# Kernel tuning notes

Hardware: AMD Instinct MI355X
Metric: run time of the kernel (lower is better)

The kernel has to match this reference:

```python
import jax, jax.numpy as jnp
import numpy as np

N, D, H, E, K = 16384, 1024, 4096, 8, 2
EPS = 1e-5


def setup_inputs() -> dict:
    key = jax.random.key(0)
    ks = jax.random.split(key, 12)
    s = 0.02
    return {
        "x": jax.random.normal(ks[0], (N, D), dtype=jnp.float32),
        "ln_g": jnp.ones((D,), jnp.float32),
        "ln_b": jnp.zeros((D,), jnp.float32),
        "r_w1": jax.random.normal(ks[1], (D, H // 2), jnp.float32) * s,
        "r_b1": jnp.zeros((H // 2,), jnp.float32),
        "r_w2": jax.random.normal(ks[2], (H // 2, E), jnp.float32) * s,
        "r_b2": jnp.zeros((E,), jnp.float32),
        "e_w1": jax.random.normal(ks[3], (E, D, H), jnp.float32) * s,
        "e_b1": jnp.zeros((E, H), jnp.float32),
        "e_w2": jax.random.normal(ks[4], (E, H, D), jnp.float32) * s,
        "e_b2": jnp.zeros((E, D), jnp.float32),
    }


def reference(x, ln_g, ln_b, r_w1, r_b1, r_w2, r_b2, e_w1, e_b1, e_w2, e_b2):
    # LayerNorm
    mu = jnp.mean(x, axis=-1, keepdims=True)
    var = jnp.mean(jnp.square(x - mu), axis=-1, keepdims=True)
    xn = (x - mu) * jax.lax.rsqrt(var + EPS) * ln_g + ln_b  # [N, D]

    # Router: Linear -> ReLU -> Linear -> softmax -> top-k, renormalize
    logits = jax.nn.relu(xn @ r_w1 + r_b1) @ r_w2 + r_b2  # [N, E]
    probs = jax.nn.softmax(logits, axis=-1)
    vals, idx = jax.lax.top_k(probs, K)  # [N, K]
    vals = vals / jnp.sum(vals, axis=-1, keepdims=True)

    # Dense expert dispatch: loop over fixed small E, weight by combine gate
    out = jnp.zeros_like(x)
    for e in range(E):
        gate = jnp.sum(vals * (idx == e).astype(vals.dtype), axis=-1)  # [N]
        h = jax.nn.relu(xn @ e_w1[e] + e_b1[e])  # dropout in eval mode -> identity
        y = h @ e_w2[e] + e_b2[e]  # [N, D]
        out = out + gate[:, None] * y
    return x + out
```

## Files before the change

kernel.cpp:

```cpp
#include <hip/hip_runtime.h>
#include <cstdint>
#include <cstddef>

typedef unsigned short u16;
typedef __attribute__((ext_vector_type(8))) short bf16x8;
typedef __attribute__((ext_vector_type(4))) float f32x4;

#define N_TOK 16384
#define DIM   1024
#define HID   4096
#define NEXP  8
#define HR    2048
#define TAU   0.02f
#define MAXMT 264

__device__ __forceinline__ u16 f2bf(float f) {
  union { float f; uint32_t u; } x; x.f = f;
  uint32_t r = x.u + 0x7FFFu + ((x.u >> 16) & 1u);
  return (u16)(r >> 16);
}
__device__ __forceinline__ float bf2f(u16 u) {
  union { uint32_t u; float f; } x; x.u = ((uint32_t)u) << 16; return x.f;
}

__device__ __forceinline__ void async16(const void* g, const void* l) {
  auto gp = reinterpret_cast<const __attribute__((address_space(1))) uint32_t*>(
      reinterpret_cast<uintptr_t>(g));
  auto lp = reinterpret_cast<__attribute__((address_space(3))) uint32_t*>(
      reinterpret_cast<uintptr_t>(l));
  __builtin_amdgcn_global_load_lds(gp, lp, 16, 0, 0);
}

__device__ __forceinline__ unsigned xcd_swz(unsigned flat, unsigned nwg) {
  const unsigned xcd = flat & 7u, lid = flat >> 3;
  const unsigned q = nwg >> 3, r = nwg & 7u;
  return (xcd < r ? xcd * (q + 1u) : r * (q + 1u) + (xcd - r) * q) + lid;
}

template<bool SPLIT>
__global__ __launch_bounds__(256)
void transpose_cvt(const float* __restrict__ src, u16* __restrict__ hi,
                   u16* __restrict__ lo, int R, int C)
{
  __shared__ float tile[32][33];
  const size_t bofs = (size_t)blockIdx.z * R * C;
  src += bofs; hi += bofs; if (SPLIT) lo += bofs;
  const int tx = threadIdx.x, ty = threadIdx.y;
  const int c0 = blockIdx.x * 32, r0 = blockIdx.y * 32;
#pragma unroll
  for (int i = 0; i < 4; ++i)
    tile[ty + i * 8][tx] = src[(size_t)(r0 + ty + i * 8) * C + c0 + tx];
  __syncthreads();
#pragma unroll
  for (int i = 0; i < 4; ++i) {
    float v = tile[tx][ty + i * 8];
    size_t o = (size_t)(c0 + ty + i * 8) * R + r0 + tx;
    u16 h = f2bf(v);
    hi[o] = h;
    if (SPLIT) lo[o] = f2bf(v - bf2f(h));
  }
}

__global__ __launch_bounds__(256)
void ln_kernel(const float* __restrict__ x, const float* __restrict__ g,
               const float* __restrict__ b, u16* __restrict__ xh,
               u16* __restrict__ xl, float* __restrict__ out)
{
  const int row = blockIdx.x;
  const int t = threadIdx.x;
  const float4 xv = ((const float4*)(x + (size_t)row * DIM))[t];
  float s = xv.x + xv.y + xv.z + xv.w;
  float q = xv.x * xv.x + xv.y * xv.y + xv.z * xv.z + xv.w * xv.w;
#pragma unroll
  for (int off = 32; off; off >>= 1) {
    s += __shfl_down(s, off, 64);
    q += __shfl_down(q, off, 64);
  }
  __shared__ float sm[8];
  __shared__ float mu_s, rs_s;
  const int lane = t & 63, wv = t >> 6;
  if (lane == 0) { sm[wv] = s; sm[wv + 4] = q; }
  __syncthreads();
  if (t == 0) {
    float S = sm[0] + sm[1] + sm[2] + sm[3];
    float Q = sm[4] + sm[5] + sm[6] + sm[7];
    float mu = S * (1.f / DIM);
    float var = Q * (1.f / DIM) - mu * mu;
    mu_s = mu; rs_s = rsqrtf(var + 1e-5f);
  }
  __syncthreads();
  const float mu = mu_s, rs = rs_s;
  const float4 gv = ((const float4*)g)[t];
  const float4 bv = ((const float4*)b)[t];
  float n0 = (xv.x - mu) * rs * gv.x + bv.x;
  float n1 = (xv.y - mu) * rs * gv.y + bv.y;
  float n2 = (xv.z - mu) * rs * gv.z + bv.z;
  float n3 = (xv.w - mu) * rs * gv.w + bv.w;
  ushort4 h, l;
  h.x = f2bf(n0); l.x = f2bf(n0 - bf2f(h.x));
  h.y = f2bf(n1); l.y = f2bf(n1 - bf2f(h.y));
  h.z = f2bf(n2); l.z = f2bf(n2 - bf2f(h.z));
  h.w = f2bf(n3); l.w = f2bf(n3 - bf2f(h.w));
  ((ushort4*)(xh + (size_t)row * DIM))[t] = h;
  ((ushort4*)(xl + (size_t)row * DIM))[t] = l;
  ((float4*)(out + (size_t)row * DIM))[t] = xv;
}

__global__ __launch_bounds__(256)
void logits_kernel(const u16* __restrict__ HrB, const float* __restrict__ w2,
                   float* __restrict__ logits)
{
  const int row = blockIdx.x, t = threadIdx.x;
  const u16* h = HrB + (size_t)row * HR;
  const ushort4* hv = (const ushort4*)(h + t * 8);
  ushort4 h0 = hv[0], h1 = hv[1];
  u16 hh[8] = {h0.x, h0.y, h0.z, h0.w, h1.x, h1.y, h1.z, h1.w};
  float p[8] = {0, 0, 0, 0, 0, 0, 0, 0};
#pragma unroll
  for (int j = 0; j < 8; ++j) {
    const int col = t * 8 + j;
    const float v = bf2f(hh[j]);
    const float4* wp = (const float4*)(w2 + (size_t)col * 8);
    float4 a = wp[0], b = wp[1];
    p[0] += v * a.x; p[1] += v * a.y; p[2] += v * a.z; p[3] += v * a.w;
    p[4] += v * b.x; p[5] += v * b.y; p[6] += v * b.z; p[7] += v * b.w;
  }
#pragma unroll
  for (int off = 32; off; off >>= 1)
#pragma unroll
    for (int e = 0; e < 8; ++e) p[e] += __shfl_down(p[e], off, 64);
  __shared__ float sm[4][8];
  const int lane = t & 63, wv = t >> 6;
  if (lane == 0) {
#pragma unroll
    for (int e = 0; e < 8; ++e) sm[wv][e] = p[e];
  }
  __syncthreads();
  if (t < 8)
    logits[(size_t)row * 8 + t] = sm[0][t] + sm[1][t] + sm[2][t] + sm[3][t];
}

__device__ __forceinline__ void load_logits(const float* logits, const float* b2,
                                            int row, float l[8]) {
  const float4* lp = (const float4*)(logits + (size_t)row * 8);
  float4 a = lp[0], b = lp[1];
  l[0] = a.x + b2[0]; l[1] = a.y + b2[1]; l[2] = a.z + b2[2]; l[3] = a.w + b2[3];
  l[4] = b.x + b2[4]; l[5] = b.y + b2[5]; l[6] = b.z + b2[6]; l[7] = b.w + b2[7];
}
__device__ __forceinline__ void top2(const float l[8], int& i0, float& l0,
                                     int& i1, float& l1) {
  i0 = 0; l0 = l[0];
#pragma unroll
  for (int e = 1; e < 8; ++e) if (l[e] > l0) { l0 = l[e]; i0 = e; }
  i1 = -1; l1 = -1e30f;
#pragma unroll
  for (int e = 0; e < 8; ++e) if (e != i0 && l[e] > l1) { l1 = l[e]; i1 = e; }
}

__global__ __launch_bounds__(256)
void pass_flag(float* __restrict__ logits, const float* __restrict__ b2,
               int* __restrict__ fixL, int* __restrict__ cntFix)
{
  __shared__ int lcnt;
  __shared__ int base;
  const int t = threadIdx.x;
  const int row = blockIdx.x * 256 + t;
  if (t == 0) lcnt = 0;
  float l[8]; load_logits(logits, b2, row, l);
  int i0, i1; float l0, l1;
  top2(l, i0, l0, i1, l1);
  float l2 = -1e30f;
#pragma unroll
  for (int e = 0; e < 8; ++e)
    if (e != i0 && e != i1 && l[e] > l2) l2 = l[e];
  const bool flag = (l1 - l2) < TAU;
  __syncthreads();
  int r = 0;
  if (flag) r = atomicAdd(&lcnt, 1);
  __syncthreads();
  if (t == 0) base = atomicAdd(cntFix, lcnt);
  __syncthreads();
  if (flag) {
    fixL[base + r] = row;
    float4 z = {0.f, 0.f, 0.f, 0.f};
    ((float4*)(logits + (size_t)row * 8))[0] = z;
    ((float4*)(logits + (size_t)row * 8))[1] = z;
  }
}

__global__ __launch_bounds__(256)
void pass_count(const float* __restrict__ logits, const float* __restrict__ b2,
                int* __restrict__ cnts)
{
  __shared__ int lcnt[NEXP];
  const int t = threadIdx.x;
  const int row = blockIdx.x * 256 + t;
  if (t < NEXP) lcnt[t] = 0;
  float l[8]; load_logits(logits, b2, row, l);
  int i0, i1; float l0, l1;
  top2(l, i0, l0, i1, l1);
  __syncthreads();
  atomicAdd(&lcnt[i0], 1);
  atomicAdd(&lcnt[i1], 1);
  __syncthreads();
  if (t < NEXP) atomicAdd(&cnts[t], lcnt[t]);
}

__global__ void scan_kernel(const int* __restrict__ cnts, int* __restrict__ offs,
                            int* __restrict__ tileOffs)
{
  if (threadIdx.x == 0) {
    int s = 0, ts = 0;
#pragma unroll
    for (int e = 0; e < NEXP; ++e) {
      offs[e] = s; s += cnts[e];
      tileOffs[e] = ts; ts += (cnts[e] + 127) >> 7;
    }
    offs[NEXP] = s;
    tileOffs[NEXP] = ts;
  }
}

__global__ __launch_bounds__(256)
void pass_scatter(const float* __restrict__ logits, const float* __restrict__ b2,
                  const int* __restrict__ offs, int* __restrict__ cnts2,
                  int* __restrict__ rowsC, float* __restrict__ gateC)
{
  __shared__ int lcnt[NEXP];
  __shared__ int sbase[NEXP];
  const int t = threadIdx.x;
  const int row = blockIdx.x * 256 + t;
  if (t < NEXP) lcnt[t] = 0;
  float l[8]; load_logits(logits, b2, row, l);
  int i0, i1; float l0, l1;
  top2(l, i0, l0, i1, l1);
  float tt = expf(l1 - l0);
  float g0 = 1.f / (1.f + tt);
  float g1 = tt / (1.f + tt);
  __syncthreads();
  int r0 = atomicAdd(&lcnt[i0], 1);
  int r1 = atomicAdd(&lcnt[i1], 1);
  __syncthreads();
  if (t < NEXP) sbase[t] = atomicAdd(&cnts2[t], lcnt[t]);
  __syncthreads();
  int p0 = offs[i0] + sbase[i0] + r0;
  int p1 = offs[i1] + sbase[i1] + r1;
  rowsC[p0] = row; gateC[p0] = g0;
  rowsC[p1] = row; gateC[p1] = g1;
}

template<int EPI, bool GATHER, bool DENSE>
__global__ __launch_bounds__(256, 3)
void gemm_moe(const u16* __restrict__ A0, const u16* __restrict__ B0,
              int lda, int ldb, int K, int NT, int Mdense,
              size_t bStrideE, int biasStrideE,
              const int* __restrict__ counts,
              const int* __restrict__ offs, const int* __restrict__ tileOffs,
              const int* __restrict__ rowsC, const float* __restrict__ gatesC,
              const float* __restrict__ bias,
              u16* __restrict__ Cbf, float* __restrict__ Cf32, int ldc)
{
  const unsigned swz = xcd_swz(blockIdx.x, gridDim.x);
  const int mt = (int)(swz / (unsigned)NT);
  int e, m0, Mq, off;
  if constexpr (DENSE) {
    if (mt >= Mdense / 128) return;
    e = 0; m0 = mt * 128; Mq = Mdense; off = 0;
  } else {
    if (mt >= tileOffs[NEXP]) return;
    e = 0;
#pragma unroll
    for (int i = 1; i < NEXP; ++i) if (tileOffs[i] <= mt) e = i;
    m0 = (mt - tileOffs[e]) * 128;
    Mq = counts[e];
    if (m0 >= Mq) return;
    off = offs[e];
  }
  const int n0 = (int)(swz % (unsigned)NT) * 128;
  const int* rows = DENSE ? nullptr : (rowsC + off);
  const u16* B = B0 + (size_t)e * bStrideE;
  const float* bi = bias + (size_t)e * biasStrideE;

  __shared__ alignas(16) u16 As[3][128 * 32];
  __shared__ alignas(16) u16 Bs[3][128 * 32];

  const int t = threadIdx.x;
  const int numK = K >> 5;

  const u16* aptr[2]; const u16* bptr[2]; int sdst[2];
#pragma unroll
  for (int i = 0; i < 2; ++i) {
    const int gdx = i * 256 + t;
    const int r = gdx >> 2;
    const int cb = ((gdx & 3) << 4) ^ (((gdx >> 5) & 1) << 5);
    const int cs = cb >> 1;
    int amc = (m0 + r) < Mq ? (m0 + r) : (Mq - 1);
    const size_t agr = DENSE ? (size_t)(m0 + r)
                             : (GATHER ? (size_t)rows[amc] : (size_t)(off + amc));
    aptr[i] = A0 + agr * lda + cs;
    bptr[i] = B + (size_t)(n0 + r) * ldb + cs;
    sdst[i] = gdx * 8;
  }

  const int lane = t & 63, wv = t >> 6;
  const int wm = wv >> 1;
  const int wn = wv & 1;
  const int fr = lane & 15, fq = lane >> 4;

  int aIdx[4], bIdx[4];
#pragma unroll
  for (int mf = 0; mf < 4; ++mf) {
    const int r = wm * 64 + mf * 16 + fr;
    aIdx[mf] = r * 32 + ((fq * 8) ^ (((r >> 3) & 1) << 4));
  }
#pragma unroll
  for (int nf = 0; nf < 4; ++nf) {
    const int rb = wn * 64 + nf * 16 + fr;
    bIdx[nf] = rb * 32 + ((fq * 8) ^ (((rb >> 3) & 1) << 4));
  }

  f32x4 acc[4][4];
#pragma unroll
  for (int i = 0; i < 4; ++i)
#pragma unroll
    for (int j = 0; j < 4; ++j) acc[i][j] = (f32x4){0.f, 0.f, 0.f, 0.f};

#pragma unroll
  for (int h = 0; h < 2; ++h) {
    async16(bptr[0] + h * 32, &Bs[h][sdst[0]]);
    async16(bptr[1] + h * 32, &Bs[h][sdst[1]]);
    async16(aptr[0] + h * 32, &As[h][sdst[0]]);
    async16(aptr[1] + h * 32, &As[h][sdst[1]]);
  }
  asm volatile("s_waitcnt vmcnt(4)" ::: "memory");
  __builtin_amdgcn_s_barrier();
  __builtin_amdgcn_sched_barrier(0);

  int sR = 0;
  int sW = 2;
  for (int T = 0; T < numK; ++T) {
    if (T + 2 < numK) {
      async16(bptr[0] + (size_t)(T + 2) * 32, &Bs[sW][sdst[0]]);
      async16(bptr[1] + (size_t)(T + 2) * 32, &Bs[sW][sdst[1]]);
      async16(aptr[0] + (size_t)(T + 2) * 32, &As[sW][sdst[0]]);
      async16(aptr[1] + (size_t)(T + 2) * 32, &As[sW][sdst[1]]);
    }

    const u16* aL = As[sR];
    const u16* bL = Bs[sR];
    bf16x8 aF[4], bF[4];
#pragma unroll
    for (int i = 0; i < 4; ++i) {
      aF[i] = *(const bf16x8*)&aL[aIdx[i]];
      bF[i] = *(const bf16x8*)&bL[bIdx[i]];
    }
    __builtin_amdgcn_s_setprio(1);
#pragma unroll
    for (int mf = 0; mf < 4; ++mf)
#pragma unroll
      for (int nf = 0; nf < 4; ++nf)
        acc[mf][nf] = __builtin_amdgcn_mfma_f32_16x16x32_bf16(
            aF[mf], bF[nf], acc[mf][nf], 0, 0, 0);
    __builtin_amdgcn_s_setprio(0);
    __builtin_amdgcn_sched_barrier(0);

    const int rem = numK - T;
    if (rem >= 3) {
      asm volatile("s_waitcnt vmcnt(4)" ::: "memory");
      __builtin_amdgcn_s_barrier();
      __builtin_amdgcn_sched_barrier(0);
    } else if (rem == 2) {
      asm volatile("s_waitcnt vmcnt(0)" ::: "memory");
      __builtin_amdgcn_s_barrier();
      __builtin_amdgcn_sched_barrier(0);
    }

    sR = (sR == 2) ? 0 : sR + 1;
    sW = (sW == 2) ? 0 : sW + 1;
  }

  float bv[4];
#pragma unroll
  for (int nf = 0; nf < 4; ++nf) bv[nf] = bi[n0 + wn * 64 + nf * 16 + fr];

#pragma unroll
  for (int mf = 0; mf < 4; ++mf)
#pragma unroll
    for (int r = 0; r < 4; ++r) {
      const int m = m0 + wm * 64 + mf * 16 + fq * 4 + r;
      if (m < Mq) {
        if constexpr (EPI == 2) {
          const size_t orow = (size_t)rows[m];
          const float g = gatesC[off + m];
#pragma unroll
          for (int nf = 0; nf < 4; ++nf) {
            const int n = n0 + wn * 64 + nf * 16 + fr;
            atomicAdd(&Cf32[orow * ldc + n], g * (acc[mf][nf][r] + bv[nf]));
          }
        } else {
#pragma unroll
          for (int nf = 0; nf < 4; ++nf) {
            const int n = n0 + wn * 64 + nf * 16 + fr;
            Cbf[(size_t)(off + m) * ldc + n] =
                f2bf(fmaxf(acc[mf][nf][r] + bv[nf], 0.f));
          }
        }
      }
    }
}

template<bool SPLIT, int EPI, bool GATHER>
__global__ __launch_bounds__(256, 2)
void gemm_bt(const u16* __restrict__ A0, const u16* __restrict__ A1,
             const u16* __restrict__ B0, const u16* __restrict__ B1,
             int lda, int ldb, int K, int M,
             const int* __restrict__ counts, int expertArg,
             const int* __restrict__ offs,
             const int* __restrict__ rowsC, const float* __restrict__ gatesC,
             const float* __restrict__ bias,
             const float* __restrict__ w2, float* __restrict__ logits,
             u16* __restrict__ Cbf, float* __restrict__ Cf32, int ldc)
{
  int expert, m0, n0;
  if (counts == nullptr) {
    const unsigned nwg = gridDim.x * gridDim.y;
    const unsigned flat = blockIdx.y * gridDim.x + blockIdx.x;
    const unsigned swz = xcd_swz(flat, nwg);
    expert = expertArg;
    m0 = (int)(swz / gridDim.x) * 128;
    n0 = (int)(swz % gridDim.x) * 128;
  } else {
    expert = expertArg;
    m0 = blockIdx.y * 128;
    n0 = blockIdx.x * 128;
  }

  const int Mq = counts ? counts[expert] : M;
  if (m0 >= Mq) return;
  const int off = offs ? offs[expert] : 0;
  const int* rows = rowsC ? rowsC + off : nullptr;
  const float* gates = gatesC ? gatesC + off : nullptr;
  const u16* B = B0;
  const u16* Bl = SPLIT ? B1 : nullptr;
  const float* bi = bias;
  const int z = (int)blockIdx.z;
  const int zOff = z * K;

  __shared__ u16 As0[128 * 32], Bs0[128 * 32];
  __shared__ u16 As1[SPLIT ? 128 * 32 : 8], Bs1[SPLIT ? 128 * 32 : 8];

  const int t = threadIdx.x;
  size_t aoff[2]; int acodd[2]; size_t boff[2];
#pragma unroll
  for (int i = 0; i < 2; ++i) {
    int gdx = i * 256 + t;
    int ar = gdx >> 2, ac = (gdx & 3) * 8;
    int am = m0 + ar;
    int amc = am < Mq ? am : (Mq - 1);
    int agr = GATHER ? rows[amc] : amc;
    aoff[i] = (size_t)agr * lda + ac + zOff;
    boff[i] = (size_t)(n0 + ar) * ldb + ac + zOff;
    acodd[i] = gdx * 8;
  }

  f32x4 acc[4][4];
#pragma unroll
  for (int i = 0; i < 4; ++i)
#pragma unroll
    for (int j = 0; j < 4; ++j) acc[i][j] = (f32x4){0.f, 0.f, 0.f, 0.f};

  const int lane = t & 63, wv = t >> 6;
  const int wm = (wv >> 1) * 64, wn = (wv & 1) * 64;
  const int fr = lane & 15, fq = lane >> 4;

  for (int k0 = 0; k0 < K; k0 += 32) {
    __syncthreads();
#pragma unroll
    for (int i = 0; i < 2; ++i) {
      async16(A0 + aoff[i] + k0, &As0[acodd[i]]);
      async16(B + boff[i] + k0, &Bs0[acodd[i]]);
      if (SPLIT) {
        async16(A1 + aoff[i] + k0, &As1[acodd[i]]);
        async16(Bl + boff[i] + k0, &Bs1[acodd[i]]);
      }
    }
    __syncthreads();
    bf16x8 af[4], bfr[4], af1[4], bf1[4];
#pragma unroll
    for (int xi = 0; xi < 4; ++xi) {
      af[xi]  = *(const bf16x8*)&As0[(wm + xi * 16 + fr) * 32 + fq * 8];
      bfr[xi] = *(const bf16x8*)&Bs0[(wn + xi * 16 + fr) * 32 + fq * 8];
      if (SPLIT) {
        af1[xi] = *(const bf16x8*)&As1[(wm + xi * 16 + fr) * 32 + fq * 8];
        bf1[xi] = *(const bf16x8*)&Bs1[(wn + xi * 16 + fr) * 32 + fq * 8];
      }
    }
#pragma unroll
    for (int mt = 0; mt < 4; ++mt)
#pragma unroll
      for (int nt = 0; nt < 4; ++nt) {
        acc[mt][nt] = __builtin_amdgcn_mfma_f32_16x16x32_bf16(af[mt], bfr[nt], acc[mt][nt], 0, 0, 0);
        if (SPLIT) {
          acc[mt][nt] = __builtin_amdgcn_mfma_f32_16x16x32_bf16(af[mt], bf1[nt], acc[mt][nt], 0, 0, 0);
          acc[mt][nt] = __builtin_amdgcn_mfma_f32_16x16x32_bf16(af1[mt], bfr[nt], acc[mt][nt], 0, 0, 0);
        }
      }
  }

  if constexpr (EPI == 3) {
    float w2v[4][8]; float b1v[4];
#pragma unroll
    for (int nt = 0; nt < 4; ++nt) {
      const int n = n0 + wn + nt * 16 + fr;
      b1v[nt] = bi[n];
      const float4* wp = (const float4*)(w2 + (size_t)n * 8);
      float4 wa = wp[0], wb = wp[1];
      w2v[nt][0] = wa.x; w2v[nt][1] = wa.y; w2v[nt][2] = wa.z; w2v[nt][3] = wa.w;
      w2v[nt][4] = wb.x; w2v[nt][5] = wb.y; w2v[nt][6] = wb.z; w2v[nt][7] = wb.w;
    }
#pragma unroll
    for (int mt = 0; mt < 4; ++mt) {
      float pe[4][8];
#pragma unroll
      for (int r = 0; r < 4; ++r)
#pragma unroll
        for (int ee = 0; ee < 8; ++ee) pe[r][ee] = 0.f;
#pragma unroll
      for (int nt = 0; nt < 4; ++nt)
#pragma unroll
        for (int r = 0; r < 4; ++r) {
          float v = fmaxf(acc[mt][nt][r] + b1v[nt], 0.f);
#pragma unroll
          for (int ee = 0; ee < 8; ++ee) pe[r][ee] += v * w2v[nt][ee];
        }
#pragma unroll
      for (int offx = 1; offx < 16; offx <<= 1)
#pragma unroll
        for (int r = 0; r < 4; ++r)
#pragma unroll
          for (int ee = 0; ee < 8; ++ee)
            pe[r][ee] += __shfl_xor(pe[r][ee], offx, 64);
      if (fr == 0) {
#pragma unroll
        for (int r = 0; r < 4; ++r) {
          const int m = m0 + wm + mt * 16 + fq * 4 + r;
          if (m < Mq) {
            const int lrow = GATHER ? rows[m] : m;
#pragma unroll
            for (int ee = 0; ee < 8; ++ee)
              atomicAdd(&logits[(size_t)lrow * 8 + ee], pe[r][ee]);
          }
        }
      }
    }
    return;
  }

#pragma unroll
  for (int mt = 0; mt < 4; ++mt) {
#pragma unroll
    for (int nt = 0; nt < 4; ++nt) {
      const int n = n0 + wn + nt * 16 + fr;
      const float bvv = (z == 0) ? bi[n] : 0.f;
#pragma unroll
      for (int r = 0; r < 4; ++r) {
        const int m = m0 + wm + mt * 16 + fq * 4 + r;
        if (m < Mq) {
          float v = acc[mt][nt][r] + bvv;
          if constexpr (EPI == 1) {
            Cbf[(size_t)m * ldc + n] = f2bf(fmaxf(v, 0.f));
          } else {
            atomicAdd(&Cf32[(size_t)rows[m] * ldc + n], gates[m] * v);
          }
        }
      }
    }
  }
}

extern "C" void kernel_launch(void* const* d_in, const int* in_sizes, int n_in,
                              void* d_out, int out_size, void* d_ws, size_t ws_size,
                              hipStream_t stream)
{
  const float* x    = (const float*)d_in[0];
  const float* ln_g = (const float*)d_in[1];
  const float* ln_b = (const float*)d_in[2];
  const float* r_w1 = (const float*)d_in[3];
  const float* r_b1 = (const float*)d_in[4];
  const float* r_w2 = (const float*)d_in[5];
  const float* r_b2 = (const float*)d_in[6];
  const float* e_w1 = (const float*)d_in[7];
  const float* e_b1 = (const float*)d_in[8];
  const float* e_w2 = (const float*)d_in[9];
  const float* e_b2 = (const float*)d_in[10];
  float* out = (float*)d_out;

  char* ws = (char*)d_ws;
  const size_t MB = 1024ull * 1024ull;
  u16*   xnhi = (u16*)(ws);
  u16*   xnlo = (u16*)(ws + 32 * MB);
  u16*   rw1h = (u16*)(ws + 64 * MB);
  u16*   rw1l = (u16*)(ws + 68 * MB);
  u16*   ew1t = (u16*)(ws + 72 * MB);
  u16*   ew2t = (u16*)(ws + 136 * MB);
  float* logits = (float*)(ws + 200 * MB);
  int*   rowsC  = (int*)(ws + 200 * MB + 512 * 1024);
  float* gateC  = (float*)(ws + 200 * MB + 640 * 1024);
  int*   fixL   = (int*)(ws + 200 * MB + 768 * 1024);
  int*   cntb   = (int*)(ws + 200 * MB + 832 * 1024);
  int*   cnts   = cntb;
  int*   cnts2  = cntb + 8;
  int*   offs   = cntb + 16;
  int*   cntFix = cntb + 25;
  int*   tileOffs = cntb + 32;
  u16*   Hbuf = (u16*)(ws + 201 * MB);
  u16*   HrB  = Hbuf;
  (void)in_sizes; (void)n_in; (void)out_size;

  const bool fused = ws_size >= 458ull * MB;

  hipMemsetAsync(cntb, 0, 256, stream);

  dim3 tb(32, 8);
  transpose_cvt<true ><<<dim3(HR / 32, DIM / 32, 1), tb, 0, stream>>>(r_w1, rw1h, rw1l, DIM, HR);
  transpose_cvt<false><<<dim3(HID / 32, DIM / 32, NEXP), tb, 0, stream>>>(e_w1, ew1t, nullptr, DIM, HID);
  transpose_cvt<false><<<dim3(DIM / 32, HID / 32, NEXP), tb, 0, stream>>>(e_w2, ew2t, nullptr, HID, DIM);

  ln_kernel<<<N_TOK, 256, 0, stream>>>(x, ln_g, ln_b, xnhi, xnlo, out);

  gemm_moe<1, false, true><<<dim3((HR / 128) * (N_TOK / 128)), 256, 0, stream>>>(
      xnhi, rw1h, DIM, DIM, DIM, HR / 128, N_TOK, 0, 0,
      nullptr, nullptr, nullptr, nullptr, nullptr, r_b1,
      HrB, nullptr, HR);

  logits_kernel<<<N_TOK, 256, 0, stream>>>(HrB, r_w2, logits);

  pass_flag<<<N_TOK / 256, 256, 0, stream>>>(logits, r_b2, fixL, cntFix);

  gemm_bt<true, 3, true><<<dim3(HR / 128, N_TOK / 128), 256, 0, stream>>>(
      xnhi, xnlo, rw1h, rw1l, DIM, DIM, DIM, N_TOK,
      cntFix, 0, nullptr, fixL, nullptr, r_b1, r_w2, logits,
      nullptr, nullptr, 0);

  pass_count<<<N_TOK / 256, 256, 0, stream>>>(logits, r_b2, cnts);
  scan_kernel<<<1, 64, 0, stream>>>(cnts, offs, tileOffs);
  pass_scatter<<<N_TOK / 256, 256, 0, stream>>>(logits, r_b2, offs, cnts2, rowsC, gateC);

  if (fused) {
    gemm_moe<1, true, false><<<dim3((HID / 128) * MAXMT), 256, 0, stream>>>(
        xnhi, ew1t, DIM, DIM, DIM, HID / 128, 0,
        (size_t)HID * DIM, HID,
        cnts, offs, tileOffs, rowsC, nullptr, e_b1,
        Hbuf, nullptr, HID);
    gemm_moe<2, false, false><<<dim3((DIM / 128) * MAXMT), 256, 0, stream>>>(
        Hbuf, ew2t, HID, HID, HID, DIM / 128, 0,
        (size_t)DIM * HID, DIM,
        cnts, offs, tileOffs, rowsC, gateC, e_b2,
        nullptr, out, DIM);
  } else {
    for (int e = 0; e < NEXP; ++e) {
      gemm_bt<false, 1, true><<<dim3(HID / 128, N_TOK / 128), 256, 0, stream>>>(
          xnhi, nullptr, ew1t + (size_t)e * HID * DIM, nullptr,
          DIM, DIM, DIM, N_TOK,
          cnts, e, offs, rowsC, nullptr, e_b1 + (size_t)e * HID, nullptr, nullptr,
          Hbuf, nullptr, HID);
      gemm_bt<false, 2, false><<<dim3(DIM / 128, N_TOK / 128, 2), 256, 0, stream>>>(
          Hbuf, nullptr, ew2t + (size_t)e * DIM * HID, nullptr,
          HID, HID, HID / 2, N_TOK,
          cnts, e, offs, rowsC, gateC, e_b2 + (size_t)e * DIM, nullptr, nullptr,
          nullptr, out, DIM);
    }
  }
}
```

Before: 1.445 ms.

## Replace 128x128 MoE GEMM with 256x256 8-wave ping-pong pipelined kernel

Swaps the 128x128-tile, 4-wave GEMM used for the router first layer and both expert GEMMs for a 256x256-tile, 512-thread kernel with K-step 64 and double-buffered LDS split into halves. The loop interleaves quarter-tile MFMA groups with async loads of the next tiles, separated by barriers, and a second tile-offset table is added for 256-row expert tiles. The aim is more data reuse per byte loaded and better overlap of loads with MFMA. The cost is more padding waste on partial expert tiles, fewer blocks in the grid, and higher register and LDS pressure.

```diff
diff --git a/kernel.cpp b/kernel.cpp
--- a/kernel.cpp
+++ b/kernel.cpp
@@ -13,6 +13,7 @@
 #define HR    2048
 #define TAU   0.02f
 #define MAXMT 264
+#define MAXMT2 136
 
 __device__ __forceinline__ u16 f2bf(float f) {
   union { float f; uint32_t u; } x; x.f = f;
@@ -207,17 +208,19 @@
 }
 
 __global__ void scan_kernel(const int* __restrict__ cnts, int* __restrict__ offs,
-                            int* __restrict__ tileOffs)
+                            int* __restrict__ tileOffs, int* __restrict__ tileOffs2)
 {
   if (threadIdx.x == 0) {
-    int s = 0, ts = 0;
+    int s = 0, ts = 0, ts2 = 0;
 #pragma unroll
     for (int e = 0; e < NEXP; ++e) {
       offs[e] = s; s += cnts[e];
       tileOffs[e] = ts; ts += (cnts[e] + 127) >> 7;
+      tileOffs2[e] = ts2; ts2 += (cnts[e] + 255) >> 8;
     }
     offs[NEXP] = s;
     tileOffs[NEXP] = ts;
+    tileOffs2[NEXP] = ts2;
   }
 }
 
@@ -249,159 +252,202 @@
   rowsC[p1] = row; gateC[p1] = g1;
 }
 
+#define G8_BAR() do { __builtin_amdgcn_s_barrier(); \
+                      __builtin_amdgcn_sched_barrier(0); } while (0)
+#define G8_VM4() asm volatile("s_waitcnt vmcnt(4)" ::: "memory")
+#define G8_VM0() asm volatile("s_waitcnt vmcnt(0)" ::: "memory")
+
+#define READ_A(aL, mfh, Af) do { \
+  _Pragma("unroll") for (int mf = 0; mf < 4; ++mf) { \
+    Af[mf][0] = *(const bf16x8*)&(aL)[((mfh)*4+mf)*1024 + aBase + swzC[0]]; \
+    Af[mf][1] = *(const bf16x8*)&(aL)[((mfh)*4+mf)*1024 + aBase + swzC[1]]; \
+  } } while (0)
+
+#define READ_B(bL, nfh, Bf) do { \
+  _Pragma("unroll") for (int nf = 0; nf < 2; ++nf) { \
+    Bf[nf][0] = *(const bf16x8*)&(bL)[((nfh)*2+nf)*1024 + bBase + swzC[0]]; \
+    Bf[nf][1] = *(const bf16x8*)&(bL)[((nfh)*2+nf)*1024 + bBase + swzC[1]]; \
+  } } while (0)
+
+#define MFMA_Q(mfh, nfh, Af, Bf) do { \
+  __builtin_amdgcn_s_setprio(1); \
+  _Pragma("unroll") for (int mf = 0; mf < 4; ++mf) \
+  _Pragma("unroll") for (int nf = 0; nf < 2; ++nf) { \
+    acc[(mfh)*4+mf][(nfh)*2+nf] = __builtin_amdgcn_mfma_f32_16x16x32_bf16( \
+        Af[mf][0], Bf[nf][0], acc[(mfh)*4+mf][(nfh)*2+nf], 0, 0, 0); \
+    acc[(mfh)*4+mf][(nfh)*2+nf] = __builtin_amdgcn_mfma_f32_16x16x32_bf16( \
+        Af[mf][1], Bf[nf][1], acc[(mfh)*4+mf][(nfh)*2+nf], 0, 0, 0); \
+  } \
+  __builtin_amdgcn_s_setprio(0); } while (0)
+
 template<int EPI, bool GATHER, bool DENSE>
-__global__ __launch_bounds__(256, 3)
-void gemm_moe(const u16* __restrict__ A0, const u16* __restrict__ B0,
-              int lda, int ldb, int K, int NT, int Mdense,
-              size_t bStrideE, int biasStrideE,
-              const int* __restrict__ counts,
-              const int* __restrict__ offs, const int* __restrict__ tileOffs,
-              const int* __restrict__ rowsC, const float* __restrict__ gatesC,
-              const float* __restrict__ bias,
-              u16* __restrict__ Cbf, float* __restrict__ Cf32, int ldc)
+__global__ __launch_bounds__(512, 2)
+void gemm8p(const u16* __restrict__ A0, const u16* __restrict__ B0,
+            int lda, int ldb, int K, int NT, int Mdense,
+            size_t bStrideE, int biasStrideE,
+            const int* __restrict__ counts, const int* __restrict__ offs,
+            const int* __restrict__ tileOffs,
+            const int* __restrict__ rowsC, const float* __restrict__ gatesC,
+            const float* __restrict__ bias,
+            u16* __restrict__ Cbf, float* __restrict__ Cf32, int ldc)
 {
   const unsigned swz = xcd_swz(blockIdx.x, gridDim.x);
   const int mt = (int)(swz / (unsigned)NT);
   int e, m0, Mq, off;
   if constexpr (DENSE) {
-    if (mt >= Mdense / 128) return;
-    e = 0; m0 = mt * 128; Mq = Mdense; off = 0;
+    if (mt >= Mdense / 256) return;
+    e = 0; m0 = mt * 256; Mq = Mdense; off = 0;
   } else {
     if (mt >= tileOffs[NEXP]) return;
     e = 0;
 #pragma unroll
     for (int i = 1; i < NEXP; ++i) if (tileOffs[i] <= mt) e = i;
-    m0 = (mt - tileOffs[e]) * 128;
+    m0 = (mt - tileOffs[e]) * 256;
     Mq = counts[e];
     if (m0 >= Mq) return;
     off = offs[e];
   }
-  const int n0 = (int)(swz % (unsigned)NT) * 128;
+  const int n0 = (int)(swz % (unsigned)NT) * 256;
   const int* rows = DENSE ? nullptr : (rowsC + off);
   const u16* B = B0 + (size_t)e * bStrideE;
   const float* bi = bias + (size_t)e * biasStrideE;
 
-  __shared__ alignas(16) u16 As[3][128 * 32];
-  __shared__ alignas(16) u16 Bs[3][128 * 32];
+  __shared__ alignas(16) u16 As[2][2][128 * 64];
+  __shared__ alignas(16) u16 Bs[2][2][128 * 64];
 
   const int t = threadIdx.x;
-  const int numK = K >> 5;
-
-  const u16* aptr[2]; const u16* bptr[2]; int sdst[2];
-#pragma unroll
-  for (int i = 0; i < 2; ++i) {
-    const int gdx = i * 256 + t;
-    const int r = gdx >> 2;
-    const int cb = ((gdx & 3) << 4) ^ (((gdx >> 5) & 1) << 5);
-    const int cs = cb >> 1;
-    int amc = (m0 + r) < Mq ? (m0 + r) : (Mq - 1);
-    const size_t agr = DENSE ? (size_t)(m0 + r)
-                             : (GATHER ? (size_t)rows[amc] : (size_t)(off + amc));
-    aptr[i] = A0 + agr * lda + cs;
-    bptr[i] = B + (size_t)(n0 + r) * ldb + cs;
-    sdst[i] = gdx * 8;
-  }
+  const int numK = K >> 6;
+
+  const u16* aP[2][2]; const u16* bP[2][2]; int dst[2];
+#pragma unroll
+  for (int j = 0; j < 2; ++j) {
+    const int gdx = j * 512 + t;
+    const int rw = gdx >> 3;
+    const int cs = ((gdx & 7) ^ (rw & 7)) << 3;
+    dst[j] = gdx * 8;
+#pragma unroll
+    for (int h = 0; h < 2; ++h) {
+      const int grow = m0 + h * 128 + rw;
+      if constexpr (DENSE) {
+        aP[h][j] = A0 + (size_t)grow * lda + cs;
+      } else {
+        const int amc = grow < Mq ? grow : (Mq - 1);
+        const size_t agr = GATHER ? (size_t)rows[amc] : (size_t)(off + amc);
+        aP[h][j] = A0 + agr * lda + cs;
+      }
+      bP[h][j] = B + (size_t)(n0 + h * 128 + rw) * ldb + cs;
+    }
+  }
+
+  auto stA = [&](int tile, int h) {
+    async16(aP[h][0] + (size_t)tile * 64, &As[tile & 1][h][dst[0]]);
+    async16(aP[h][1] + (size_t)tile * 64, &As[tile & 1][h][dst[1]]);
+  };
+  auto stB = [&](int tile, int h) {
+    async16(bP[h][0] + (size_t)tile * 64, &Bs[tile & 1][h][dst[0]]);
+    async16(bP[h][1] + (size_t)tile * 64, &Bs[tile & 1][h][dst[1]]);
+  };
 
   const int lane = t & 63, wv = t >> 6;
-  const int wm = wv >> 1;
-  const int wn = wv & 1;
+  const int wr = wv >> 2;
+  const int wc = wv & 3;
   const int fr = lane & 15, fq = lane >> 4;
 
-  int aIdx[4], bIdx[4];
-#pragma unroll
-  for (int mf = 0; mf < 4; ++mf) {
-    const int r = wm * 64 + mf * 16 + fr;
-    aIdx[mf] = r * 32 + ((fq * 8) ^ (((r >> 3) & 1) << 4));
-  }
-#pragma unroll
-  for (int nf = 0; nf < 4; ++nf) {
-    const int rb = wn * 64 + nf * 16 + fr;
-    bIdx[nf] = rb * 32 + ((fq * 8) ^ (((rb >> 3) & 1) << 4));
-  }
-
-  f32x4 acc[4][4];
-#pragma unroll
-  for (int i = 0; i < 4; ++i)
+  int swzC[2];
+#pragma unroll
+  for (int ks = 0; ks < 2; ++ks)
+    swzC[ks] = ((ks * 4 + fq) ^ (fr & 7)) << 3;
+  const int aBase = fr * 64;
+  const int bBase = (wc & 1) * 4096 + fr * 64;
+
+  const u16* aH[2] = { &As[0][wr][0], &As[1][wr][0] };
+  const u16* bH[2] = { &Bs[0][wc >> 1][0], &Bs[1][wc >> 1][0] };
+
+  f32x4 acc[8][4];
+#pragma unroll
+  for (int i = 0; i < 8; ++i)
 #pragma unroll
     for (int j = 0; j < 4; ++j) acc[i][j] = (f32x4){0.f, 0.f, 0.f, 0.f};
 
-#pragma unroll
-  for (int h = 0; h < 2; ++h) {
-    async16(bptr[0] + h * 32, &Bs[h][sdst[0]]);
-    async16(bptr[1] + h * 32, &Bs[h][sdst[1]]);
-    async16(aptr[0] + h * 32, &As[h][sdst[0]]);
-    async16(aptr[1] + h * 32, &As[h][sdst[1]]);
-  }
-  asm volatile("s_waitcnt vmcnt(4)" ::: "memory");
-  __builtin_amdgcn_s_barrier();
-  __builtin_amdgcn_sched_barrier(0);
-
-  int sR = 0;
-  int sW = 2;
-  for (int T = 0; T < numK; ++T) {
-    if (T + 2 < numK) {
-      async16(bptr[0] + (size_t)(T + 2) * 32, &Bs[sW][sdst[0]]);
-      async16(bptr[1] + (size_t)(T + 2) * 32, &Bs[sW][sdst[1]]);
-      async16(aptr[0] + (size_t)(T + 2) * 32, &As[sW][sdst[0]]);
-      async16(aptr[1] + (size_t)(T + 2) * 32, &As[sW][sdst[1]]);
-    }
-
-    const u16* aL = As[sR];
-    const u16* bL = Bs[sR];
-    bf16x8 aF[4], bF[4];
-#pragma unroll
-    for (int i = 0; i < 4; ++i) {
-      aF[i] = *(const bf16x8*)&aL[aIdx[i]];
-      bF[i] = *(const bf16x8*)&bL[bIdx[i]];
-    }
-    __builtin_amdgcn_s_setprio(1);
-#pragma unroll
-    for (int mf = 0; mf < 4; ++mf)
-#pragma unroll
-      for (int nf = 0; nf < 4; ++nf)
-        acc[mf][nf] = __builtin_amdgcn_mfma_f32_16x16x32_bf16(
-            aF[mf], bF[nf], acc[mf][nf], 0, 0, 0);
-    __builtin_amdgcn_s_setprio(0);
-    __builtin_amdgcn_sched_barrier(0);
-
-    const int rem = numK - T;
-    if (rem >= 3) {
-      asm volatile("s_waitcnt vmcnt(4)" ::: "memory");
-      __builtin_amdgcn_s_barrier();
-      __builtin_amdgcn_sched_barrier(0);
-    } else if (rem == 2) {
-      asm volatile("s_waitcnt vmcnt(0)" ::: "memory");
-      __builtin_amdgcn_s_barrier();
-      __builtin_amdgcn_sched_barrier(0);
-    }
-
-    sR = (sR == 2) ? 0 : sR + 1;
-    sW = (sW == 2) ? 0 : sW + 1;
+  stB(0, 0); stB(0, 1); stA(0, 0); stA(0, 1);
+  stB(1, 0); stB(1, 1);
+  G8_VM4();
+  G8_BAR();
+
+  bf16x8 Af[4][2], Bf0[2][2], Bf1[2][2];
+
+  const int numI = numK >> 1;
+  for (int it = 0; it < numI; ++it) {
+    const int t1 = 2 * it + 1, t2 = 2 * it + 2, t3 = 2 * it + 3;
+    const bool last = (t2 >= numK);
+    READ_A(aH[0], 0, Af);
+    READ_B(bH[0], 0, Bf0);
+    stA(t1, 0);
+    G8_BAR();
+    MFMA_Q(0, 0, Af, Bf0);
+    G8_BAR();
+    READ_B(bH[0], 1, Bf1);
+    stA(t1, 1);
+    G8_BAR();
+    MFMA_Q(0, 1, Af, Bf1);
+    G8_BAR();
+    READ_A(aH[0], 1, Af);
+    if (!last) stB(t2, 0);
+    G8_BAR();
+    MFMA_Q(1, 1, Af, Bf1);
+    G8_BAR();
+    if (!last) stB(t2, 1);
+    G8_BAR();
+    MFMA_Q(1, 0, Af, Bf0);
+    if (last) { G8_VM0(); } else { G8_VM4(); }
+    G8_BAR();
+    READ_A(aH[1], 0, Af);
+    READ_B(bH[1], 0, Bf0);
+    if (!last) stA(t2, 0);
+    G8_BAR();
+    MFMA_Q(0, 0, Af, Bf0);
+    G8_BAR();
+    READ_B(bH[1], 1, Bf1);
+    if (!last) stA(t2, 1);
+    G8_BAR();
+    MFMA_Q(0, 1, Af, Bf1);
+    G8_BAR();
+    READ_A(aH[1], 1, Af);
+    if (t3 < numK) stB(t3, 0);
+    G8_BAR();
+    MFMA_Q(1, 1, Af, Bf1);
+    G8_BAR();
+    if (t3 < numK) stB(t3, 1);
+    G8_BAR();
+    MFMA_Q(1, 0, Af, Bf0);
+    if (!last) { G8_VM4(); }
+    G8_BAR();
   }
 
   float bv[4];
 #pragma unroll
-  for (int nf = 0; nf < 4; ++nf) bv[nf] = bi[n0 + wn * 64 + nf * 16 + fr];
-
-#pragma unroll
-  for (int mf = 0; mf < 4; ++mf)
+  for (int nf = 0; nf < 4; ++nf) bv[nf] = bi[n0 + wc * 64 + nf * 16 + fr];
+
+  const int crowBase = DENSE ? 0 : off;
+#pragma unroll
+  for (int mf = 0; mf < 8; ++mf)
 #pragma unroll
     for (int r = 0; r < 4; ++r) {
-      const int m = m0 + wm * 64 + mf * 16 + fq * 4 + r;
+      const int m = m0 + wr * 128 + mf * 16 + fq * 4 + r;
       if (m < Mq) {
         if constexpr (EPI == 2) {
           const size_t orow = (size_t)rows[m];
           const float g = gatesC[off + m];
 #pragma unroll
           for (int nf = 0; nf < 4; ++nf) {
-            const int n = n0 + wn * 64 + nf * 16 + fr;
+            const int n = n0 + wc * 64 + nf * 16 + fr;
             atomicAdd(&Cf32[orow * ldc + n], g * (acc[mf][nf][r] + bv[nf]));
           }
         } else {
 #pragma unroll
           for (int nf = 0; nf < 4; ++nf) {
-            const int n = n0 + wn * 64 + nf * 16 + fr;
-            Cbf[(size_t)(off + m) * ldc + n] =
+            const int n = n0 + wc * 64 + nf * 16 + fr;
+            Cbf[(size_t)(crowBase + m) * ldc + n] =
                 f2bf(fmaxf(acc[mf][nf][r] + bv[nf], 0.f));
           }
         }
@@ -612,7 +658,8 @@
   int*   cnts2  = cntb + 8;
   int*   offs   = cntb + 16;
   int*   cntFix = cntb + 25;
-  int*   tileOffs = cntb + 32;
+  int*   tileOffs  = cntb + 32;
+  int*   tileOffs2 = cntb + 48;
   u16*   Hbuf = (u16*)(ws + 201 * MB);
   u16*   HrB  = Hbuf;
   (void)in_sizes; (void)n_in; (void)out_size;
@@ -628,8 +675,8 @@
 
   ln_kernel<<<N_TOK, 256, 0, stream>>>(x, ln_g, ln_b, xnhi, xnlo, out);
 
-  gemm_moe<1, false, true><<<dim3((HR / 128) * (N_TOK / 128)), 256, 0, stream>>>(
-      xnhi, rw1h, DIM, DIM, DIM, HR / 128, N_TOK, 0, 0,
+  gemm8p<1, false, true><<<dim3((HR / 256) * (N_TOK / 256)), 512, 0, stream>>>(
+      xnhi, rw1h, DIM, DIM, DIM, HR / 256, N_TOK, 0, 0,
       nullptr, nullptr, nullptr, nullptr, nullptr, r_b1,
       HrB, nullptr, HR);
 
@@ -643,19 +690,19 @@
       nullptr, nullptr, 0);
 
   pass_count<<<N_TOK / 256, 256, 0, stream>>>(logits, r_b2, cnts);
-  scan_kernel<<<1, 64, 0, stream>>>(cnts, offs, tileOffs);
+  scan_kernel<<<1, 64, 0, stream>>>(cnts, offs, tileOffs, tileOffs2);
   pass_scatter<<<N_TOK / 256, 256, 0, stream>>>(logits, r_b2, offs, cnts2, rowsC, gateC);
 
   if (fused) {
-    gemm_moe<1, true, false><<<dim3((HID / 128) * MAXMT), 256, 0, stream>>>(
-        xnhi, ew1t, DIM, DIM, DIM, HID / 128, 0,
+    gemm8p<1, true, false><<<dim3((HID / 256) * MAXMT2), 512, 0, stream>>>(
+        xnhi, ew1t, DIM, DIM, DIM, HID / 256, 0,
         (size_t)HID * DIM, HID,
-        cnts, offs, tileOffs, rowsC, nullptr, e_b1,
+        cnts, offs, tileOffs2, rowsC, nullptr, e_b1,
         Hbuf, nullptr, HID);
-    gemm_moe<2, false, false><<<dim3((DIM / 128) * MAXMT), 256, 0, stream>>>(
-        Hbuf, ew2t, HID, HID, HID, DIM / 128, 0,
+    gemm8p<2, false, false><<<dim3((DIM / 256) * MAXMT2), 512, 0, stream>>>(
+        Hbuf, ew2t, HID, HID, HID, DIM / 256, 0,
         (size_t)DIM * HID, DIM,
-        cnts, offs, tileOffs, rowsC, gateC, e_b2,
+        cnts, offs, tileOffs2, rowsC, gateC, e_b2,
         nullptr, out, DIM);
   } else {
     for (int e = 0; e < NEXP; ++e) {
```

After: 1.363 ms. 1.06x faster.
